# Performance work log

Measured on AMD Instinct MI355X. Metric: run time of the kernel, lower is better.

## Reference

```python
import jax, jax.numpy as jnp
import numpy as np

NUM_GROUPS = 32
EPS = 1e-6


def setup_inputs() -> dict:
    key = jax.random.key(0)
    ks = jax.random.split(key, 6)
    b, c, H, W = 4, 512, 64, 64
    scale = 1.0 / np.sqrt(c)
    return {
        "x": jax.random.normal(ks[0], (b, c, H, W), dtype=jnp.float32),
        "gn_w": jnp.ones((c,), jnp.float32),
        "gn_b": jnp.zeros((c,), jnp.float32),
        "wq": jax.random.normal(ks[1], (c, c), jnp.float32) * scale,
        "bq": jnp.zeros((c,), jnp.float32),
        "wk": jax.random.normal(ks[2], (c, c), jnp.float32) * scale,
        "bk": jnp.zeros((c,), jnp.float32),
        "wv": jax.random.normal(ks[3], (c, c), jnp.float32) * scale,
        "bv": jnp.zeros((c,), jnp.float32),
        "wp": jax.random.normal(ks[4], (c, c), jnp.float32) * scale,
        "bp": jnp.zeros((c,), jnp.float32),
    }


def _group_norm(x, gamma, beta):
    b, c, H, W = x.shape
    xg = x.reshape(b, NUM_GROUPS, c // NUM_GROUPS, H, W)
    mean = xg.mean(axis=(2, 3, 4), keepdims=True)
    var = xg.var(axis=(2, 3, 4), keepdims=True)
    xn = (xg - mean) * jax.lax.rsqrt(var + EPS)
    xn = xn.reshape(b, c, H, W)
    return xn * gamma[None, :, None, None] + beta[None, :, None, None]


def reference(x, gn_w, gn_b, wq, bq, wk, bk, wv, bv, wp, bp):
    b, c, H, W = x.shape
    h = _group_norm(x, gn_w, gn_b)  # (b,c,H,W)
    hf = h.reshape(b, c, H * W)  # (b,c,n)
    # 1x1 convs == per-pixel linear maps; weight layout [out,in]
    q = jnp.einsum('oc,bcn->bno', wq, hf) + bq  # (b,n,c)
    k = jnp.einsum('oc,bcn->bon', wk, hf) + bk[None, :, None]  # (b,c,n)
    v = jnp.einsum('oc,bcn->bon', wv, hf) + bv[None, :, None]  # (b,c,n)
    attn = jnp.einsum('bnc,bcm->bnm', q, k) * (int(c) ** (-0.5))
    attn = jax.nn.softmax(attn, axis=2)  # softmax over keys m
    # A = v @ attn^T  -> (b,c,n) where A[:, :, n] = sum_m v[:,:,m] attn[n,m]
    A = jnp.einsum('bcm,bnm->bcn', v, attn)
    A = jnp.einsum('oc,bcn->bon', wp, A) + bp[None, :, None]
    return x + A.reshape(b, c, H, W)
```

## Files before the change

kernel.cpp:

```cpp
#include <hip/hip_runtime.h>

#define BATCH 4
#define CCH 512
#define NPIX 4096
#define NGRP 32
#define GSZ 16
#define GN_EPS 1e-6f

typedef __attribute__((ext_vector_type(8))) short short8;
typedef __attribute__((ext_vector_type(8))) unsigned short ushort8;
typedef __attribute__((ext_vector_type(4))) unsigned short ushort4v;
typedef __attribute__((ext_vector_type(4))) float f32x4;

__device__ inline unsigned short f2bf(float f) {
  unsigned u = __float_as_uint(f);
  unsigned r = u + 0x7fffu + ((u >> 16) & 1u);
  return (unsigned short)(r >> 16);
}
__device__ inline float bf2f(unsigned short us) {
  return __uint_as_float(((unsigned)us) << 16);
}

__global__ __launch_bounds__(256) void gn_stats(const float* __restrict__ x,
                                                float* __restrict__ stats) {
  int bg = blockIdx.x;
  const f32x4* base = (const f32x4*)(x + (size_t)bg * (GSZ * NPIX));
  float s = 0.f, ss = 0.f;
  const int n4 = GSZ * NPIX / 4;
  for (int i = threadIdx.x; i < n4; i += 256) {
    f32x4 v = base[i];
    s += v.x + v.y + v.z + v.w;
    ss += v.x * v.x + v.y * v.y + v.z * v.z + v.w * v.w;
  }
  for (int off = 32; off > 0; off >>= 1) {
    s += __shfl_xor(s, off, 64);
    ss += __shfl_xor(ss, off, 64);
  }
  __shared__ float rs[4], rss[4];
  int lane = threadIdx.x & 63, wid = threadIdx.x >> 6;
  if (lane == 0) { rs[wid] = s; rss[wid] = ss; }
  __syncthreads();
  if (threadIdx.x == 0) {
    float S = rs[0] + rs[1] + rs[2] + rs[3];
    float SS = rss[0] + rss[1] + rss[2] + rss[3];
    const float inv = 1.f / (float)(GSZ * NPIX);
    float mean = S * inv;
    float var = SS * inv - mean * mean;
    stats[bg * 2] = mean;
    stats[bg * 2 + 1] = rsqrtf(var + GN_EPS);
  }
}

__global__ __launch_bounds__(256) void gn_apply_t(const float* __restrict__ x,
                                                  const float* __restrict__ stats,
                                                  const float* __restrict__ gw,
                                                  const float* __restrict__ gb,
                                                  unsigned short* __restrict__ hT) {
  __shared__ float tile[64][65];
  int b = blockIdx.z, c0 = blockIdx.y * 64, n0 = blockIdx.x * 64;
  int t = threadIdx.x;
  int tc4 = t & 15, tr = t >> 4;
  const float* xb = x + ((size_t)b * CCH + c0) * NPIX + n0;
#pragma unroll
  for (int j = 0; j < 4; ++j) {
    int row = tr + j * 16;
    int c = c0 + row;
    float mean = stats[((size_t)b * NGRP + (c >> 4)) * 2];
    float rstd = stats[((size_t)b * NGRP + (c >> 4)) * 2 + 1];
    float ga = gw[c] * rstd;
    float be = gb[c] - mean * ga;
    f32x4 v = *(const f32x4*)(xb + (size_t)row * NPIX + tc4 * 4);
    tile[row][tc4 * 4 + 0] = v.x * ga + be;
    tile[row][tc4 * 4 + 1] = v.y * ga + be;
    tile[row][tc4 * 4 + 2] = v.z * ga + be;
    tile[row][tc4 * 4 + 3] = v.w * ga + be;
  }
  __syncthreads();
  int cc = t & 7, nr = t >> 3;
  unsigned short* outp = hT + ((size_t)b * NPIX + n0) * CCH + c0;
#pragma unroll
  for (int j = 0; j < 2; ++j) {
    int n = nr + j * 32;
    ushort8 pk;
#pragma unroll
    for (int i = 0; i < 8; ++i) pk[i] = f2bf(tile[cc * 8 + i][n]);
    *(ushort8*)(outp + (size_t)n * CCH + cc * 8) = pk;
  }
}

__global__ __launch_bounds__(256) void f32_to_bf16(const float* __restrict__ src,
                                                   unsigned short* __restrict__ dst,
                                                   int n4) {
  int i = blockIdx.x * 256 + threadIdx.x;
  if (i < n4) {
    f32x4 v = ((const f32x4*)src)[i];
    ushort4v o;
    o.x = f2bf(v.x); o.y = f2bf(v.y); o.z = f2bf(v.z); o.w = f2bf(v.w);
    ((ushort4v*)dst)[i] = o;
  }
}

template <int BIAS_MODE, int OUT_BF16, int RESID, int SWZ>
__global__ __launch_bounds__(256, 2) void gemm_bt(
    const unsigned short* __restrict__ A, const unsigned short* __restrict__ B,
    void* __restrict__ Cv, const float* __restrict__ bias,
    const float* __restrict__ resid, int M, int N, int K, int lda, int ldb,
    int ldc, long sA, long sB, long sC, long sR, float scale) {
  __shared__ __align__(16) unsigned short lA[128][40];
  __shared__ __align__(16) unsigned short lB[128][40];
  const int t = threadIdx.x;
  const int lane = t & 63, w = t >> 6;
  const int wr = w >> 1, wc = w & 1;
  const int fr = lane & 15, kg = lane >> 4;

  unsigned orig = blockIdx.x + gridDim.x * (blockIdx.y + gridDim.y * blockIdx.z);
  unsigned nwg = gridDim.x * gridDim.y * gridDim.z;
  unsigned tid = (orig & 7) * (nwg >> 3) + (orig >> 3);
  int mt, ntl, bz;
  if (SWZ == 2) {
    unsigned bx = tid % gridDim.x, r = tid / gridDim.x;
    ntl = (int)bx;
    mt = (int)(r % gridDim.y);
    bz = (int)(r / gridDim.y);
  } else {
    unsigned bx = tid % gridDim.x, r = tid / gridDim.x;
    mt = (int)bx;
    ntl = (int)(r % gridDim.y);
    bz = (int)(r / gridDim.y);
  }
  const int m0 = mt * 128, n0 = ntl * 128;

  const unsigned short* Abz = A + (long)bz * sA;
  const unsigned short* Bbz = B + (long)bz * sB;
  const int srow = t >> 1, skc = (t & 1) * 16;
  const unsigned short* gA = Abz + (size_t)(m0 + srow) * lda + skc;
  const unsigned short* gB = Bbz + (size_t)(n0 + srow) * ldb + skc;

  short8 a0X = *(const short8*)(gA);
  short8 a1X = *(const short8*)(gA + 8);
  short8 b0X = *(const short8*)(gB);
  short8 b1X = *(const short8*)(gB + 8);
  short8 a0Y = *(const short8*)(gA + 32);
  short8 a1Y = *(const short8*)(gA + 40);
  short8 b0Y = *(const short8*)(gB + 32);
  short8 b1Y = *(const short8*)(gB + 40);

  f32x4 acc[4][4];
  const f32x4 zero = {0.f, 0.f, 0.f, 0.f};
#pragma unroll
  for (int m = 0; m < 4; ++m)
#pragma unroll
    for (int n = 0; n < 4; ++n) acc[m][n] = zero;

  const int NT = K >> 5;
#define COMPUTE()                                                             \
  do {                                                                        \
    short8 af[4], bfr[4];                                                     \
    _Pragma("unroll") for (int m = 0; m < 4; ++m) af[m] =                     \
        *(const short8*)&lA[wr * 64 + m * 16 + fr][kg * 8];                   \
    _Pragma("unroll") for (int n = 0; n < 4; ++n) bfr[n] =                    \
        *(const short8*)&lB[wc * 64 + n * 16 + fr][kg * 8];                   \
    _Pragma("unroll") for (int m = 0; m < 4; ++m)                             \
        _Pragma("unroll") for (int n = 0; n < 4; ++n) acc[m][n] =             \
            __builtin_amdgcn_mfma_f32_16x16x32_bf16(af[m], bfr[n],            \
                                                    acc[m][n], 0, 0, 0);      \
  } while (0)

  for (int it = 0; it < NT; it += 2) {
    __syncthreads();
    *(short8*)&lA[srow][skc] = a0X;
    *(short8*)&lA[srow][skc + 8] = a1X;
    *(short8*)&lB[srow][skc] = b0X;
    *(short8*)&lB[srow][skc + 8] = b1X;
    if (it + 2 < NT) {
      a0X = *(const short8*)(gA + (it + 2) * 32);
      a1X = *(const short8*)(gA + (it + 2) * 32 + 8);
      b0X = *(const short8*)(gB + (it + 2) * 32);
      b1X = *(const short8*)(gB + (it + 2) * 32 + 8);
    }
    __syncthreads();
    COMPUTE();
    __syncthreads();
    *(short8*)&lA[srow][skc] = a0Y;
    *(short8*)&lA[srow][skc + 8] = a1Y;
    *(short8*)&lB[srow][skc] = b0Y;
    *(short8*)&lB[srow][skc + 8] = b1Y;
    if (it + 3 < NT) {
      a0Y = *(const short8*)(gA + (it + 3) * 32);
      a1Y = *(const short8*)(gA + (it + 3) * 32 + 8);
      b0Y = *(const short8*)(gB + (it + 3) * 32);
      b1Y = *(const short8*)(gB + (it + 3) * 32 + 8);
    }
    __syncthreads();
    COMPUTE();
  }
#undef COMPUTE

  const int rowbase = m0 + wr * 64 + kg * 4;
  const int colbase = n0 + wc * 64 + fr;
#pragma unroll
  for (int m = 0; m < 4; ++m) {
#pragma unroll
    for (int n = 0; n < 4; ++n) {
      int col = colbase + n * 16;
#pragma unroll
      for (int r = 0; r < 4; ++r) {
        int row = rowbase + m * 16 + r;
        float v = acc[m][n][r] * scale;
        if (BIAS_MODE == 1) v += bias[row];
        if (BIAS_MODE == 2) v += bias[col];
        if (RESID) v += resid[(size_t)bz * sR + (size_t)row * ldc + col];
        size_t idx = (size_t)bz * sC + (size_t)row * ldc + col;
        if (OUT_BF16)
          ((unsigned short*)Cv)[idx] = f2bf(v);
        else
          ((float*)Cv)[idx] = v;
      }
    }
  }
}

__global__ __launch_bounds__(512, 2) void attn_fused(
    const unsigned short* __restrict__ qg, const unsigned short* __restrict__ kgl,
    const unsigned short* __restrict__ vg, unsigned short* __restrict__ og,
    float scale) {
  __shared__ __align__(16) unsigned short Qs[64 * 512];
  __shared__ __align__(16) unsigned short Ck[2][16384];
  __shared__ __align__(16) unsigned short Ps[64 * 128];
  __shared__ float lred[2][32][4];
  __shared__ float linv[64];

  const int t = threadIdx.x;
  const int lane = t & 63;
  const int wid = t >> 6;
  const int wq = wid >> 2, wc = wid & 3;
  const int fr = lane & 15, kgp = lane >> 4;

  unsigned logical = ((unsigned)blockIdx.x & 7) * 32 + ((unsigned)blockIdx.x >> 3);
  const int bz = (int)(logical >> 6), qt = (int)(logical & 63);
  const size_t BS = (size_t)NPIX * CCH;
  const unsigned short* qb = qg + (size_t)bz * BS + (size_t)qt * 64 * CCH;
  const unsigned short* kb = kgl + (size_t)bz * BS;
  const unsigned short* vb = vg + (size_t)bz * BS;

  {
    const int row = t >> 3, c0 = (t & 7) * 64;
    const unsigned short* src = qb + (size_t)row * CCH + c0;
    const int sw = (row & 7) << 3;
#pragma unroll
    for (int i = 0; i < 8; ++i)
      *(short8*)&Qs[row * 512 + ((c0 + i * 8) ^ sw)] = *(const short8*)(src + i * 8);
  }

  const int krow = t >> 2, kseg = t & 3;
  const int kswz = (krow & 7) << 3;
  const unsigned short* gK = kb + (size_t)krow * CCH + kseg * 32;
  const unsigned short* gV = vb + (size_t)t * NPIX;

  short8 R0, R1, R2, R3;
#define LOADK(mt_, cc_)                                                       \
  do { const unsigned short* g = gK + (size_t)(mt_) * (128 * CCH) + (cc_) * 128; \
    R0 = *(const short8*)(g); R1 = *(const short8*)(g + 8);                   \
    R2 = *(const short8*)(g + 16); R3 = *(const short8*)(g + 24); } while (0)
#define LOADV(mt_, vc_)                                                       \
  do { const unsigned short* g = gV + (mt_) * 128 + (vc_) * 32;               \
    R0 = *(const short8*)(g); R1 = *(const short8*)(g + 8);                   \
    R2 = *(const short8*)(g + 16); R3 = *(const short8*)(g + 24); } while (0)
#define WRITEK(buf_)                                                          \
  do { unsigned short* d = &Ck[buf_][krow * 128];                             \
    *(short8*)(d + ((kseg * 32 + 0) ^ kswz)) = R0;                            \
    *(short8*)(d + ((kseg * 32 + 8) ^ kswz)) = R1;                            \
    *(short8*)(d + ((kseg * 32 + 16) ^ kswz)) = R2;                           \
    *(short8*)(d + ((kseg * 32 + 24) ^ kswz)) = R3; } while (0)
#define WRITEV(buf_)                                                          \
  do { unsigned short* d = &Ck[buf_][t * 8];                                  \
    *(short8*)(d + 0 * 4096) = R0; *(short8*)(d + 1 * 4096) = R1;             \
    *(short8*)(d + 2 * 4096) = R2; *(short8*)(d + 3 * 4096) = R3; } while (0)

#define PHASE_BAR()                                                           \
  do {                                                                        \
    __builtin_amdgcn_sched_barrier(0);                                        \
    asm volatile("s_waitcnt lgkmcnt(0)" ::: "memory");                        \
    __builtin_amdgcn_s_barrier();                                             \
    __builtin_amdgcn_sched_barrier(0);                                        \
  } while (0)

  f32x4 oa[2][8];
  const f32x4 zero = {0.f, 0.f, 0.f, 0.f};
#pragma unroll
  for (int i = 0; i < 2; ++i)
#pragma unroll
    for (int j = 0; j < 8; ++j) oa[i][j] = zero;
  f32x4 racc0 = zero, racc1 = zero;

  LOADK(0, 0);
  for (int mt = 0; mt < 32; ++mt) {
    f32x4 s00 = zero, s01 = zero, s10 = zero, s11 = zero;
#pragma unroll
    for (int ph = 0; ph < 8; ++ph) {
      const int buf = ph & 1;
      if (ph < 4) WRITEK(buf); else WRITEV(buf);
      if (ph < 3) { LOADK(mt, ph + 1); }
      else if (ph == 3) { LOADV(mt, 0); }
      else if (ph < 7) { LOADV(mt, ph - 3); }
      else { if (mt + 1 < 32) LOADK(mt + 1, 0); }
      PHASE_BAR();
      if (ph < 4) {
        __builtin_amdgcn_s_setprio(1);
#pragma unroll
        for (int kk = 0; kk < 4; ++kk) {
          const int q0 = wq * 32 + fr, q1 = wq * 32 + 16 + fr;
          const int col = ph * 128 + kk * 32 + kgp * 8;
          short8 a0 = *(const short8*)&Qs[q0 * 512 + ((col) ^ ((q0 & 7) << 3))];
          short8 a1 = *(const short8*)&Qs[q1 * 512 + ((col) ^ ((q1 & 7) << 3))];
          const int m0r = wc * 32 + fr, m1r = wc * 32 + 16 + fr;
          short8 b0 = *(const short8*)&Ck[buf][m0r * 128 +
                      ((kk * 32 + kgp * 8) ^ ((m0r & 7) << 3))];
          short8 b1 = *(const short8*)&Ck[buf][m1r * 128 +
                      ((kk * 32 + kgp * 8) ^ ((m1r & 7) << 3))];
          s00 = __builtin_amdgcn_mfma_f32_16x16x32_bf16(a0, b0, s00, 0, 0, 0);
          s01 = __builtin_amdgcn_mfma_f32_16x16x32_bf16(a0, b1, s01, 0, 0, 0);
          s10 = __builtin_amdgcn_mfma_f32_16x16x32_bf16(a1, b0, s10, 0, 0, 0);
          s11 = __builtin_amdgcn_mfma_f32_16x16x32_bf16(a1, b1, s11, 0, 0, 0);
        }
        __builtin_amdgcn_s_setprio(0);
        if (ph == 3) {
          f32x4 p00, p01, p10, p11;
#pragma unroll
          for (int r = 0; r < 4; ++r) {
            p00[r] = __expf(s00[r] * scale);
            p01[r] = __expf(s01[r] * scale);
            p10[r] = __expf(s10[r] * scale);
            p11[r] = __expf(s11[r] * scale);
          }
          f32x4 rs0 = p00 + p01, rs1 = p10 + p11;
#pragma unroll
          for (int off = 1; off <= 8; off <<= 1) {
#pragma unroll
            for (int r = 0; r < 4; ++r) {
              rs0[r] += __shfl_xor(rs0[r], off, 64);
              rs1[r] += __shfl_xor(rs1[r], off, 64);
            }
          }
          racc0 += rs0;
          racc1 += rs1;
#pragma unroll
          for (int r = 0; r < 4; ++r) {
            const int qa = wq * 32 + kgp * 4 + r;
            const int qbr = wq * 32 + 16 + kgp * 4 + r;
            const int swa = (qa & 7) << 3, swb = (qbr & 7) << 3;
            Ps[qa * 128 + ((wc * 32 + fr) ^ swa)] = f2bf(p00[r]);
            Ps[qa * 128 + ((wc * 32 + 16 + fr) ^ swa)] = f2bf(p01[r]);
            Ps[qbr * 128 + ((wc * 32 + fr) ^ swb)] = f2bf(p10[r]);
            Ps[qbr * 128 + ((wc * 32 + 16 + fr) ^ swb)] = f2bf(p11[r]);
          }
        }
      } else {
        const int vc = ph - 4;
        const int q0 = wq * 32 + fr, q1 = wq * 32 + 16 + fr;
        short8 pa0 = *(const short8*)&Ps[q0 * 128 +
                     ((vc * 32 + kgp * 8) ^ ((q0 & 7) << 3))];
        short8 pa1 = *(const short8*)&Ps[q1 * 128 +
                     ((vc * 32 + kgp * 8) ^ ((q1 & 7) << 3))];
        __builtin_amdgcn_s_setprio(1);
#pragma unroll
        for (int fb = 0; fb < 8; ++fb) {
          const int c = wc * 128 + fb * 16 + fr;
          short8 bv = *(const short8*)&Ck[buf][kgp * 4096 + c * 8];
          oa[0][fb] = __builtin_amdgcn_mfma_f32_16x16x32_bf16(pa0, bv, oa[0][fb], 0, 0, 0);
          oa[1][fb] = __builtin_amdgcn_mfma_f32_16x16x32_bf16(pa1, bv, oa[1][fb], 0, 0, 0);
        }
        __builtin_amdgcn_s_setprio(0);
      }
    }
  }
#undef LOADK
#undef LOADV
#undef WRITEK
#undef WRITEV
#undef PHASE_BAR

  __syncthreads();
  if (fr == 0) {
#pragma unroll
    for (int r = 0; r < 4; ++r) {
      lred[wq][kgp * 4 + r][wc] = racc0[r];
      lred[wq][16 + kgp * 4 + r][wc] = racc1[r];
    }
  }
  __syncthreads();
  if (t < 64) {
    float s = lred[t >> 5][t & 31][0] + lred[t >> 5][t & 31][1] +
              lred[t >> 5][t & 31][2] + lred[t >> 5][t & 31][3];
    linv[t] = 1.f / s;
  }
  __syncthreads();
#pragma unroll
  for (int i = 0; i < 2; ++i) {
    f32x4 li = *(const f32x4*)&linv[wq * 32 + i * 16 + kgp * 4];
#pragma unroll
    for (int fb = 0; fb < 8; ++fb) {
#pragma unroll
      for (int r = 0; r < 4; ++r) {
        const int q = wq * 32 + i * 16 + kgp * 4 + r;
        const int col = wc * 128 + fb * 16 + fr;
        Qs[q * 512 + (col ^ ((q & 7) << 3))] = f2bf(oa[i][fb][r] * li[r]);
      }
    }
  }
  __syncthreads();
  {
    const int row = t >> 3, c0 = (t & 7) * 64;
    const int sw = (row & 7) << 3;
    unsigned short* dst = og + (size_t)bz * BS + ((size_t)qt * 64 + row) * CCH + c0;
#pragma unroll
    for (int i = 0; i < 8; ++i)
      *(short8*)(dst + i * 8) = *(const short8*)&Qs[row * 512 + ((c0 + i * 8) ^ sw)];
  }
}

extern "C" void kernel_launch(void* const* d_in, const int* in_sizes, int n_in,
                              void* d_out, int out_size, void* d_ws, size_t ws_size,
                              hipStream_t stream) {
  const float* x = (const float*)d_in[0];
  const float* gnw = (const float*)d_in[1];
  const float* gnb = (const float*)d_in[2];
  const float* wq = (const float*)d_in[3];
  const float* bq = (const float*)d_in[4];
  const float* wk = (const float*)d_in[5];
  const float* bk = (const float*)d_in[6];
  const float* wv = (const float*)d_in[7];
  const float* bv = (const float*)d_in[8];
  const float* wp = (const float*)d_in[9];
  const float* bp = (const float*)d_in[10];
  float* out = (float*)d_out;

  const size_t BS = (size_t)NPIX * CCH;

  char* ws = (char*)d_ws;
  float* stats = (float*)ws;
  unsigned short* hT = (unsigned short*)(ws + 1024);
  unsigned short* Abuf = hT;
  unsigned short* qb = hT + BATCH * BS;
  unsigned short* kTb = qb + BATCH * BS;
  unsigned short* vb = kTb + BATCH * BS;
  unsigned short* wqb = vb + BATCH * BS;
  unsigned short* wkb = wqb + CCH * CCH;
  unsigned short* wvb = wkb + CCH * CCH;
  unsigned short* wpb = wvb + CCH * CCH;
  size_t need = (size_t)((char*)(wpb + CCH * CCH) - ws);
  if (ws_size < need) return;

  f32_to_bf16<<<256, 256, 0, stream>>>(wq, wqb, CCH * CCH / 4);
  f32_to_bf16<<<256, 256, 0, stream>>>(wk, wkb, CCH * CCH / 4);
  f32_to_bf16<<<256, 256, 0, stream>>>(wv, wvb, CCH * CCH / 4);
  f32_to_bf16<<<256, 256, 0, stream>>>(wp, wpb, CCH * CCH / 4);

  gn_stats<<<BATCH * NGRP, 256, 0, stream>>>(x, stats);
  gn_apply_t<<<dim3(NPIX / 64, CCH / 64, BATCH), 256, 0, stream>>>(x, stats, gnw,
                                                                   gnb, hT);

  gemm_bt<2, 1, 0, 2><<<dim3(4, 32, BATCH), 256, 0, stream>>>(
      hT, wqb, qb, bq, nullptr, NPIX, CCH, CCH, CCH, CCH, CCH, (long)BS, 0,
      (long)BS, 0, 1.f);
  gemm_bt<2, 1, 0, 2><<<dim3(4, 32, BATCH), 256, 0, stream>>>(
      hT, wkb, kTb, bk, nullptr, NPIX, CCH, CCH, CCH, CCH, CCH, (long)BS, 0,
      (long)BS, 0, 1.f);
  gemm_bt<1, 1, 0, 0><<<dim3(4, 32, BATCH), 256, 0, stream>>>(
      wvb, hT, vb, bv, nullptr, CCH, NPIX, CCH, CCH, CCH, NPIX, 0, (long)BS,
      (long)BS, 0, 1.f);

  const float sscale = 0.044194173824159216f;
  attn_fused<<<BATCH * 64, 512, 0, stream>>>(qb, kTb, vb, Abuf, sscale);

  gemm_bt<1, 0, 1, 0><<<dim3(4, 32, BATCH), 256, 0, stream>>>(
      wpb, Abuf, out, bp, x, CCH, NPIX, CCH, CCH, CCH, NPIX, 0, (long)BS,
      (long)BS, (long)BS, 1.f);
}
```

Measured before the change: 336.3 us.

## Shrink attention query tile to 32 rows with 256-thread blocks

Restructures the fused attention kernel to process 32 query rows per block with 4 waves instead of 64 rows with 8 waves, launching 512 blocks instead of 256. Each wave now owns a 32-key slice for QK^T and a 64-channel slice (in two halves) for PV, with K staged in 64-channel chunks and V staged in 8 smaller phases. The aim is to fill more CUs with less LDS per block. The cost is that K/V tiles are reloaded from global or L2 twice as often in total, and there are more barriers per tile.

```diff
diff --git a/kernel.cpp b/kernel.cpp
--- a/kernel.cpp
+++ b/kernel.cpp
@@ -220,62 +220,54 @@
   }
 }
 
-__global__ __launch_bounds__(512, 2) void attn_fused(
+__global__ __launch_bounds__(256, 2) void attn_fused(
     const unsigned short* __restrict__ qg, const unsigned short* __restrict__ kgl,
     const unsigned short* __restrict__ vg, unsigned short* __restrict__ og,
     float scale) {
-  __shared__ __align__(16) unsigned short Qs[64 * 512];
-  __shared__ __align__(16) unsigned short Ck[2][16384];
-  __shared__ __align__(16) unsigned short Ps[64 * 128];
-  __shared__ float lred[2][32][4];
-  __shared__ float linv[64];
+  __shared__ __align__(16) unsigned short Qs[32 * 512];
+  __shared__ __align__(16) unsigned short Ck[2][8192];
+  __shared__ __align__(16) unsigned short Ps[32 * 128];
+  __shared__ float lred[32][4];
+  __shared__ float linv[32];
 
   const int t = threadIdx.x;
   const int lane = t & 63;
-  const int wid = t >> 6;
-  const int wq = wid >> 2, wc = wid & 3;
+  const int w = t >> 6;
   const int fr = lane & 15, kgp = lane >> 4;
 
-  unsigned logical = ((unsigned)blockIdx.x & 7) * 32 + ((unsigned)blockIdx.x >> 3);
-  const int bz = (int)(logical >> 6), qt = (int)(logical & 63);
+  unsigned logical = ((unsigned)blockIdx.x & 7) * 64 + ((unsigned)blockIdx.x >> 3);
+  const int bz = (int)(logical >> 7), qt = (int)(logical & 127);
   const size_t BS = (size_t)NPIX * CCH;
-  const unsigned short* qb = qg + (size_t)bz * BS + (size_t)qt * 64 * CCH;
+  const unsigned short* qb = qg + (size_t)bz * BS + (size_t)qt * 32 * CCH;
   const unsigned short* kb = kgl + (size_t)bz * BS;
   const unsigned short* vb = vg + (size_t)bz * BS;
 
-  {
-    const int row = t >> 3, c0 = (t & 7) * 64;
-    const unsigned short* src = qb + (size_t)row * CCH + c0;
-    const int sw = (row & 7) << 3;
-#pragma unroll
-    for (int i = 0; i < 8; ++i)
-      *(short8*)&Qs[row * 512 + ((c0 + i * 8) ^ sw)] = *(const short8*)(src + i * 8);
-  }
-
-  const int krow = t >> 2, kseg = t & 3;
-  const int kswz = (krow & 7) << 3;
-  const unsigned short* gK = kb + (size_t)krow * CCH + kseg * 32;
+  const int krow = t >> 1;
+  const int kch4 = (t & 1) * 4;
+  const int kswz = krow & 7;
+  const unsigned short* gK = kb + (size_t)krow * CCH + (t & 1) * 32;
   const unsigned short* gV = vb + (size_t)t * NPIX;
 
   short8 R0, R1, R2, R3;
-#define LOADK(mt_, cc_)                                                       \
-  do { const unsigned short* g = gK + (size_t)(mt_) * (128 * CCH) + (cc_) * 128; \
+#define LOADK(mt_, sub_)                                                      \
+  do { const unsigned short* g = gK + (size_t)(mt_) * (128 * CCH) + (sub_) * 64; \
     R0 = *(const short8*)(g); R1 = *(const short8*)(g + 8);                   \
     R2 = *(const short8*)(g + 16); R3 = *(const short8*)(g + 24); } while (0)
-#define LOADV(mt_, vc_)                                                       \
-  do { const unsigned short* g = gV + (mt_) * 128 + (vc_) * 32;               \
+#define LOADV(mt_, vph_)                                                      \
+  do { const unsigned short* g = gV + (size_t)((vph_) & 1) * (256 * NPIX) +   \
+        (mt_) * 128 + ((vph_) >> 1) * 32;                                     \
     R0 = *(const short8*)(g); R1 = *(const short8*)(g + 8);                   \
     R2 = *(const short8*)(g + 16); R3 = *(const short8*)(g + 24); } while (0)
 #define WRITEK(buf_)                                                          \
-  do { unsigned short* d = &Ck[buf_][krow * 128];                             \
-    *(short8*)(d + ((kseg * 32 + 0) ^ kswz)) = R0;                            \
-    *(short8*)(d + ((kseg * 32 + 8) ^ kswz)) = R1;                            \
-    *(short8*)(d + ((kseg * 32 + 16) ^ kswz)) = R2;                           \
-    *(short8*)(d + ((kseg * 32 + 24) ^ kswz)) = R3; } while (0)
+  do { unsigned short* d = &Ck[buf_][krow * 64];                              \
+    *(short8*)(d + (((kch4 + 0) ^ kswz) << 3)) = R0;                          \
+    *(short8*)(d + (((kch4 + 1) ^ kswz) << 3)) = R1;                          \
+    *(short8*)(d + (((kch4 + 2) ^ kswz) << 3)) = R2;                          \
+    *(short8*)(d + (((kch4 + 3) ^ kswz) << 3)) = R3; } while (0)
 #define WRITEV(buf_)                                                          \
   do { unsigned short* d = &Ck[buf_][t * 8];                                  \
-    *(short8*)(d + 0 * 4096) = R0; *(short8*)(d + 1 * 4096) = R1;             \
-    *(short8*)(d + 2 * 4096) = R2; *(short8*)(d + 3 * 4096) = R3; } while (0)
+    *(short8*)(d + 0 * 2048) = R0; *(short8*)(d + 1 * 2048) = R1;             \
+    *(short8*)(d + 2 * 2048) = R2; *(short8*)(d + 3 * 2048) = R3; } while (0)
 
 #define PHASE_BAR()                                                           \
   do {                                                                        \
@@ -285,93 +277,123 @@
     __builtin_amdgcn_sched_barrier(0);                                        \
   } while (0)
 
-  f32x4 oa[2][8];
+  LOADK(0, 0);
+  {
+    const int row = t >> 3, c0 = (t & 7) * 64;
+    const unsigned short* src = qb + (size_t)row * CCH + c0;
+    const int sw = (row & 7) << 3;
+#pragma unroll
+    for (int i = 0; i < 8; ++i)
+      *(short8*)&Qs[row * 512 + ((c0 + i * 8) ^ sw)] = *(const short8*)(src + i * 8);
+  }
+
+  f32x4 s_acc[2][2], o_acc[2][2][4], racc[2];
   const f32x4 zero = {0.f, 0.f, 0.f, 0.f};
 #pragma unroll
-  for (int i = 0; i < 2; ++i)
-#pragma unroll
-    for (int j = 0; j < 8; ++j) oa[i][j] = zero;
-  f32x4 racc0 = zero, racc1 = zero;
-
-  LOADK(0, 0);
+  for (int i = 0; i < 2; ++i) {
+    racc[i] = zero;
+#pragma unroll
+    for (int n = 0; n < 2; ++n) s_acc[i][n] = zero;
+#pragma unroll
+    for (int h = 0; h < 2; ++h)
+#pragma unroll
+      for (int n = 0; n < 4; ++n) o_acc[h][i][n] = zero;
+  }
+
+  short8 pa[2];
+
   for (int mt = 0; mt < 32; ++mt) {
-    f32x4 s00 = zero, s01 = zero, s10 = zero, s11 = zero;
-#pragma unroll
-    for (int ph = 0; ph < 8; ++ph) {
-      const int buf = ph & 1;
-      if (ph < 4) WRITEK(buf); else WRITEV(buf);
-      if (ph < 3) { LOADK(mt, ph + 1); }
-      else if (ph == 3) { LOADV(mt, 0); }
-      else if (ph < 7) { LOADV(mt, ph - 3); }
-      else { if (mt + 1 < 32) LOADK(mt + 1, 0); }
+#pragma unroll
+    for (int sub = 0; sub < 8; ++sub) {
+      const int buf = sub & 1;
+      WRITEK(buf);
+      if (sub < 7) LOADK(mt, sub + 1);
+      else         LOADV(mt, 0);
       PHASE_BAR();
-      if (ph < 4) {
-        __builtin_amdgcn_s_setprio(1);
-#pragma unroll
-        for (int kk = 0; kk < 4; ++kk) {
-          const int q0 = wq * 32 + fr, q1 = wq * 32 + 16 + fr;
-          const int col = ph * 128 + kk * 32 + kgp * 8;
-          short8 a0 = *(const short8*)&Qs[q0 * 512 + ((col) ^ ((q0 & 7) << 3))];
-          short8 a1 = *(const short8*)&Qs[q1 * 512 + ((col) ^ ((q1 & 7) << 3))];
-          const int m0r = wc * 32 + fr, m1r = wc * 32 + 16 + fr;
-          short8 b0 = *(const short8*)&Ck[buf][m0r * 128 +
-                      ((kk * 32 + kgp * 8) ^ ((m0r & 7) << 3))];
-          short8 b1 = *(const short8*)&Ck[buf][m1r * 128 +
-                      ((kk * 32 + kgp * 8) ^ ((m1r & 7) << 3))];
-          s00 = __builtin_amdgcn_mfma_f32_16x16x32_bf16(a0, b0, s00, 0, 0, 0);
-          s01 = __builtin_amdgcn_mfma_f32_16x16x32_bf16(a0, b1, s01, 0, 0, 0);
-          s10 = __builtin_amdgcn_mfma_f32_16x16x32_bf16(a1, b0, s10, 0, 0, 0);
-          s11 = __builtin_amdgcn_mfma_f32_16x16x32_bf16(a1, b1, s11, 0, 0, 0);
+      __builtin_amdgcn_s_setprio(1);
+#pragma unroll
+      for (int kk = 0; kk < 2; ++kk) {
+        short8 a[2], b[2];
+#pragma unroll
+        for (int i = 0; i < 2; ++i) {
+          const int q = i * 16 + fr;
+          const int col = sub * 64 + kk * 32 + kgp * 8;
+          a[i] = *(const short8*)&Qs[q * 512 + (col ^ ((q & 7) << 3))];
         }
-        __builtin_amdgcn_s_setprio(0);
-        if (ph == 3) {
-          f32x4 p00, p01, p10, p11;
+#pragma unroll
+        for (int n = 0; n < 2; ++n) {
+          const int m = w * 32 + n * 16 + fr;
+          b[n] = *(const short8*)&Ck[buf][m * 64 +
+                 (((kk * 4 + kgp) ^ (m & 7)) << 3)];
+        }
+#pragma unroll
+        for (int i = 0; i < 2; ++i)
+#pragma unroll
+          for (int n = 0; n < 2; ++n)
+            s_acc[i][n] = __builtin_amdgcn_mfma_f32_16x16x32_bf16(
+                a[i], b[n], s_acc[i][n], 0, 0, 0);
+      }
+      __builtin_amdgcn_s_setprio(0);
+      if (sub == 7) {
+#pragma unroll
+        for (int i = 0; i < 2; ++i) {
+          f32x4 p0, p1;
 #pragma unroll
           for (int r = 0; r < 4; ++r) {
-            p00[r] = __expf(s00[r] * scale);
-            p01[r] = __expf(s01[r] * scale);
-            p10[r] = __expf(s10[r] * scale);
-            p11[r] = __expf(s11[r] * scale);
+            p0[r] = __expf(s_acc[i][0][r] * scale);
+            p1[r] = __expf(s_acc[i][1][r] * scale);
           }
-          f32x4 rs0 = p00 + p01, rs1 = p10 + p11;
-#pragma unroll
-          for (int off = 1; off <= 8; off <<= 1) {
-#pragma unroll
-            for (int r = 0; r < 4; ++r) {
-              rs0[r] += __shfl_xor(rs0[r], off, 64);
-              rs1[r] += __shfl_xor(rs1[r], off, 64);
-            }
+          f32x4 rs = p0 + p1;
+#pragma unroll
+          for (int off = 1; off <= 8; off <<= 1)
+#pragma unroll
+            for (int r = 0; r < 4; ++r) rs[r] += __shfl_xor(rs[r], off, 64);
+          racc[i] += rs;
+#pragma unroll
+          for (int r = 0; r < 4; ++r) {
+            const int q = i * 16 + kgp * 4 + r;
+            const int m0e = w * 32 + fr;
+            const int m1e = w * 32 + 16 + fr;
+            Ps[q * 128 + ((((m0e >> 3) ^ (q & 7)) << 3) + (m0e & 7))] = f2bf(p0[r]);
+            Ps[q * 128 + ((((m1e >> 3) ^ (q & 7)) << 3) + (m1e & 7))] = f2bf(p1[r]);
           }
-          racc0 += rs0;
-          racc1 += rs1;
-#pragma unroll
-          for (int r = 0; r < 4; ++r) {
-            const int qa = wq * 32 + kgp * 4 + r;
-            const int qbr = wq * 32 + 16 + kgp * 4 + r;
-            const int swa = (qa & 7) << 3, swb = (qbr & 7) << 3;
-            Ps[qa * 128 + ((wc * 32 + fr) ^ swa)] = f2bf(p00[r]);
-            Ps[qa * 128 + ((wc * 32 + 16 + fr) ^ swa)] = f2bf(p01[r]);
-            Ps[qbr * 128 + ((wc * 32 + fr) ^ swb)] = f2bf(p10[r]);
-            Ps[qbr * 128 + ((wc * 32 + 16 + fr) ^ swb)] = f2bf(p11[r]);
-          }
+          s_acc[i][0] = zero;
+          s_acc[i][1] = zero;
         }
-      } else {
-        const int vc = ph - 4;
-        const int q0 = wq * 32 + fr, q1 = wq * 32 + 16 + fr;
-        short8 pa0 = *(const short8*)&Ps[q0 * 128 +
-                     ((vc * 32 + kgp * 8) ^ ((q0 & 7) << 3))];
-        short8 pa1 = *(const short8*)&Ps[q1 * 128 +
-                     ((vc * 32 + kgp * 8) ^ ((q1 & 7) << 3))];
-        __builtin_amdgcn_s_setprio(1);
-#pragma unroll
-        for (int fb = 0; fb < 8; ++fb) {
-          const int c = wc * 128 + fb * 16 + fr;
-          short8 bv = *(const short8*)&Ck[buf][kgp * 4096 + c * 8];
-          oa[0][fb] = __builtin_amdgcn_mfma_f32_16x16x32_bf16(pa0, bv, oa[0][fb], 0, 0, 0);
-          oa[1][fb] = __builtin_amdgcn_mfma_f32_16x16x32_bf16(pa1, bv, oa[1][fb], 0, 0, 0);
+      }
+    }
+#pragma unroll
+    for (int vph = 0; vph < 8; ++vph) {
+      const int buf = vph & 1;
+      const int h = vph & 1, mc = vph >> 1;
+      WRITEV(buf);
+      if (vph < 7) LOADV(mt, vph + 1);
+      else if (mt + 1 < 32) LOADK(mt + 1, 0);
+      PHASE_BAR();
+      if (h == 0) {
+#pragma unroll
+        for (int i = 0; i < 2; ++i) {
+          const int q = i * 16 + fr;
+          pa[i] = *(const short8*)&Ps[q * 128 +
+                  (((mc * 4 + kgp) ^ (q & 7)) << 3)];
         }
-        __builtin_amdgcn_s_setprio(0);
       }
+      __builtin_amdgcn_s_setprio(1);
+      {
+        short8 b[4];
+#pragma unroll
+        for (int n = 0; n < 4; ++n) {
+          const int cl = w * 64 + n * 16 + fr;
+          b[n] = *(const short8*)&Ck[buf][(kgp << 11) + cl * 8];
+        }
+#pragma unroll
+        for (int i = 0; i < 2; ++i)
+#pragma unroll
+          for (int n = 0; n < 4; ++n)
+            o_acc[h][i][n] = __builtin_amdgcn_mfma_f32_16x16x32_bf16(
+                pa[i], b[n], o_acc[h][i][n], 0, 0, 0);
+      }
+      __builtin_amdgcn_s_setprio(0);
     }
   }
 #undef LOADK
@@ -383,28 +405,30 @@
   __syncthreads();
   if (fr == 0) {
 #pragma unroll
-    for (int r = 0; r < 4; ++r) {
-      lred[wq][kgp * 4 + r][wc] = racc0[r];
-      lred[wq][16 + kgp * 4 + r][wc] = racc1[r];
-    }
+    for (int i = 0; i < 2; ++i)
+#pragma unroll
+      for (int r = 0; r < 4; ++r)
+        lred[i * 16 + kgp * 4 + r][w] = racc[i][r];
   }
   __syncthreads();
-  if (t < 64) {
-    float s = lred[t >> 5][t & 31][0] + lred[t >> 5][t & 31][1] +
-              lred[t >> 5][t & 31][2] + lred[t >> 5][t & 31][3];
+  if (t < 32) {
+    float s = lred[t][0] + lred[t][1] + lred[t][2] + lred[t][3];
     linv[t] = 1.f / s;
   }
   __syncthreads();
 #pragma unroll
   for (int i = 0; i < 2; ++i) {
-    f32x4 li = *(const f32x4*)&linv[wq * 32 + i * 16 + kgp * 4];
-#pragma unroll
-    for (int fb = 0; fb < 8; ++fb) {
-#pragma unroll
-      for (int r = 0; r < 4; ++r) {
-        const int q = wq * 32 + i * 16 + kgp * 4 + r;
-        const int col = wc * 128 + fb * 16 + fr;
-        Qs[q * 512 + (col ^ ((q & 7) << 3))] = f2bf(oa[i][fb][r] * li[r]);
+    f32x4 li = *(const f32x4*)&linv[i * 16 + kgp * 4];
+#pragma unroll
+    for (int h = 0; h < 2; ++h) {
+#pragma unroll
+      for (int n = 0; n < 4; ++n) {
+#pragma unroll
+        for (int r = 0; r < 4; ++r) {
+          const int q = i * 16 + kgp * 4 + r;
+          const int c = h * 256 + w * 64 + n * 16 + fr;
+          Qs[q * 512 + (c ^ ((q & 7) << 3))] = f2bf(o_acc[h][i][n][r] * li[r]);
+        }
       }
     }
   }
@@ -412,7 +436,7 @@
   {
     const int row = t >> 3, c0 = (t & 7) * 64;
     const int sw = (row & 7) << 3;
-    unsigned short* dst = og + (size_t)bz * BS + ((size_t)qt * 64 + row) * CCH + c0;
+    unsigned short* dst = og + (size_t)bz * BS + ((size_t)qt * 32 + row) * CCH + c0;
 #pragma unroll
     for (int i = 0; i < 8; ++i)
       *(short8*)(dst + i * 8) = *(const short8*)&Qs[row * 512 + ((c0 + i * 8) ^ sw)];
@@ -471,7 +495,7 @@
       (long)BS, 0, 1.f);
 
   const float sscale = 0.044194173824159216f;
-  attn_fused<<<BATCH * 64, 512, 0, stream>>>(qb, kTb, vb, Abuf, sscale);
+  attn_fused<<<512, 256, 0, stream>>>(qb, kTb, vb, Abuf, sscale);
 
   gemm_bt<1, 0, 1, 0><<<dim3(4, 32, BATCH), 256, 0, stream>>>(
       wpb, Abuf, out, bp, x, CCH, NPIX, CCH, CCH, CCH, NPIX, 0, (long)BS,
```

Result: slower. 457.5 us (+36.0%).

## Double attention block to 1024 threads with one 16-row query slice per wave

Applied to the files above, without the earlier changes.

The fused attention kernel now launches 1024 threads (16 waves) per block instead of 512, and each wave handles 16 query rows rather than 32, halving per-wave accumulators and MFMA work. K/V staging loads are redistributed so each thread moves two 16-byte chunks per phase instead of four, and the first K prefetch is issued before the Q tile load. The row-sum scratch now reuses the Ps buffer to save LDS. The aim is more latency hiding and less register pressure per wave. The cost is more waves per barrier, each doing less MFMA work between barriers, and the same LDS footprint, which limits blocks per CU.

```diff
diff --git a/kernel.cpp b/kernel.cpp
--- a/kernel.cpp
+++ b/kernel.cpp
@@ -220,20 +220,19 @@
   }
 }
 
-__global__ __launch_bounds__(512, 2) void attn_fused(
+__global__ __launch_bounds__(1024, 4) void attn_fused(
     const unsigned short* __restrict__ qg, const unsigned short* __restrict__ kgl,
     const unsigned short* __restrict__ vg, unsigned short* __restrict__ og,
     float scale) {
   __shared__ __align__(16) unsigned short Qs[64 * 512];
   __shared__ __align__(16) unsigned short Ck[2][16384];
   __shared__ __align__(16) unsigned short Ps[64 * 128];
-  __shared__ float lred[2][32][4];
-  __shared__ float linv[64];
 
   const int t = threadIdx.x;
   const int lane = t & 63;
   const int wid = t >> 6;
-  const int wq = wid >> 2, wc = wid & 3;
+  const int wq = wid >> 2;
+  const int wc = wid & 3;
   const int fr = lane & 15, kgp = lane >> 4;
 
   unsigned logical = ((unsigned)blockIdx.x & 7) * 32 + ((unsigned)blockIdx.x >> 3);
@@ -243,39 +242,27 @@
   const unsigned short* kb = kgl + (size_t)bz * BS;
   const unsigned short* vb = vg + (size_t)bz * BS;
 
-  {
-    const int row = t >> 3, c0 = (t & 7) * 64;
-    const unsigned short* src = qb + (size_t)row * CCH + c0;
-    const int sw = (row & 7) << 3;
-#pragma unroll
-    for (int i = 0; i < 8; ++i)
-      *(short8*)&Qs[row * 512 + ((c0 + i * 8) ^ sw)] = *(const short8*)(src + i * 8);
-  }
-
-  const int krow = t >> 2, kseg = t & 3;
-  const int kswz = (krow & 7) << 3;
-  const unsigned short* gK = kb + (size_t)krow * CCH + kseg * 32;
-  const unsigned short* gV = vb + (size_t)t * NPIX;
-
-  short8 R0, R1, R2, R3;
-#define LOADK(mt_, cc_)                                                       \
-  do { const unsigned short* g = gK + (size_t)(mt_) * (128 * CCH) + (cc_) * 128; \
-    R0 = *(const short8*)(g); R1 = *(const short8*)(g + 8);                   \
-    R2 = *(const short8*)(g + 16); R3 = *(const short8*)(g + 24); } while (0)
+  const int krow = t >> 3, kg0 = (t & 7) * 2;
+  const int kx = krow & 7;
+  const unsigned short* gKbase = kb + (size_t)krow * CCH + kg0 * 8;
+  const int vgr = t >> 8, vc0 = (2 * t) & 511;
+  const unsigned short* gV0 = vb + (size_t)vc0 * NPIX + vgr * 8;
+  const unsigned short* gV1 = vb + (size_t)(vc0 + 1) * NPIX + vgr * 8;
+
+  short8 R0, R1;
+#define LOADK(mt_, ph_)                                                       \
+  do { const unsigned short* g = gKbase + (size_t)(mt_) * (128 * CCH) + (ph_)*128; \
+    R0 = *(const short8*)(g); R1 = *(const short8*)(g + 8); } while (0)
 #define LOADV(mt_, vc_)                                                       \
-  do { const unsigned short* g = gV + (mt_) * 128 + (vc_) * 32;               \
-    R0 = *(const short8*)(g); R1 = *(const short8*)(g + 8);                   \
-    R2 = *(const short8*)(g + 16); R3 = *(const short8*)(g + 24); } while (0)
+  do { const long m0v = (long)(mt_)*128 + (long)(vc_)*32;                     \
+    R0 = *(const short8*)(gV0 + m0v); R1 = *(const short8*)(gV1 + m0v); } while (0)
 #define WRITEK(buf_)                                                          \
   do { unsigned short* d = &Ck[buf_][krow * 128];                             \
-    *(short8*)(d + ((kseg * 32 + 0) ^ kswz)) = R0;                            \
-    *(short8*)(d + ((kseg * 32 + 8) ^ kswz)) = R1;                            \
-    *(short8*)(d + ((kseg * 32 + 16) ^ kswz)) = R2;                           \
-    *(short8*)(d + ((kseg * 32 + 24) ^ kswz)) = R3; } while (0)
+    *(short8*)(d + ((kg0 ^ kx) << 3)) = R0;                                   \
+    *(short8*)(d + (((kg0 + 1) ^ kx) << 3)) = R1; } while (0)
 #define WRITEV(buf_)                                                          \
-  do { unsigned short* d = &Ck[buf_][t * 8];                                  \
-    *(short8*)(d + 0 * 4096) = R0; *(short8*)(d + 1 * 4096) = R1;             \
-    *(short8*)(d + 2 * 4096) = R2; *(short8*)(d + 3 * 4096) = R3; } while (0)
+  do { unsigned short* d = &Ck[buf_][vgr * 4096 + vc0 * 8];                   \
+    *(short8*)(d) = R0; *(short8*)(d + 8) = R1; } while (0)
 
 #define PHASE_BAR()                                                           \
   do {                                                                        \
@@ -285,90 +272,84 @@
     __builtin_amdgcn_sched_barrier(0);                                        \
   } while (0)
 
-  f32x4 oa[2][8];
+  LOADK(0, 0);
+  {
+    const int row = t >> 4, c0 = (t & 15) * 32;
+    const unsigned short* src = qb + (size_t)row * CCH + c0;
+    const int sw = (row & 7) << 3;
+#pragma unroll
+    for (int i = 0; i < 4; ++i)
+      *(short8*)&Qs[row * 512 + ((c0 + i * 8) ^ sw)] = *(const short8*)(src + i * 8);
+  }
+
+  f32x4 s_acc[2], oa[8], racc;
   const f32x4 zero = {0.f, 0.f, 0.f, 0.f};
-#pragma unroll
-  for (int i = 0; i < 2; ++i)
-#pragma unroll
-    for (int j = 0; j < 8; ++j) oa[i][j] = zero;
-  f32x4 racc0 = zero, racc1 = zero;
-
-  LOADK(0, 0);
+  s_acc[0] = zero; s_acc[1] = zero; racc = zero;
+#pragma unroll
+  for (int j = 0; j < 8; ++j) oa[j] = zero;
+
   for (int mt = 0; mt < 32; ++mt) {
-    f32x4 s00 = zero, s01 = zero, s10 = zero, s11 = zero;
 #pragma unroll
     for (int ph = 0; ph < 8; ++ph) {
       const int buf = ph & 1;
       if (ph < 4) WRITEK(buf); else WRITEV(buf);
-      if (ph < 3) { LOADK(mt, ph + 1); }
-      else if (ph == 3) { LOADV(mt, 0); }
-      else if (ph < 7) { LOADV(mt, ph - 3); }
+      if (ph < 3)       LOADK(mt, ph + 1);
+      else if (ph == 3) LOADV(mt, 0);
+      else if (ph < 7)  LOADV(mt, ph - 3);
       else { if (mt + 1 < 32) LOADK(mt + 1, 0); }
       PHASE_BAR();
       if (ph < 4) {
+        const int q0 = wq * 16 + fr;
+        const int qx = (q0 & 7) << 3;
+        const int m0r = wc * 32 + fr, m1r = wc * 32 + 16 + fr;
+        const int mx0 = (m0r & 7) << 3, mx1 = (m1r & 7) << 3;
         __builtin_amdgcn_s_setprio(1);
 #pragma unroll
         for (int kk = 0; kk < 4; ++kk) {
-          const int q0 = wq * 32 + fr, q1 = wq * 32 + 16 + fr;
           const int col = ph * 128 + kk * 32 + kgp * 8;
-          short8 a0 = *(const short8*)&Qs[q0 * 512 + ((col) ^ ((q0 & 7) << 3))];
-          short8 a1 = *(const short8*)&Qs[q1 * 512 + ((col) ^ ((q1 & 7) << 3))];
-          const int m0r = wc * 32 + fr, m1r = wc * 32 + 16 + fr;
+          short8 a = *(const short8*)&Qs[q0 * 512 + (col ^ qx)];
           short8 b0 = *(const short8*)&Ck[buf][m0r * 128 +
-                      ((kk * 32 + kgp * 8) ^ ((m0r & 7) << 3))];
+                      ((kk * 32 + kgp * 8) ^ mx0)];
           short8 b1 = *(const short8*)&Ck[buf][m1r * 128 +
-                      ((kk * 32 + kgp * 8) ^ ((m1r & 7) << 3))];
-          s00 = __builtin_amdgcn_mfma_f32_16x16x32_bf16(a0, b0, s00, 0, 0, 0);
-          s01 = __builtin_amdgcn_mfma_f32_16x16x32_bf16(a0, b1, s01, 0, 0, 0);
-          s10 = __builtin_amdgcn_mfma_f32_16x16x32_bf16(a1, b0, s10, 0, 0, 0);
-          s11 = __builtin_amdgcn_mfma_f32_16x16x32_bf16(a1, b1, s11, 0, 0, 0);
+                      ((kk * 32 + kgp * 8) ^ mx1)];
+          s_acc[0] = __builtin_amdgcn_mfma_f32_16x16x32_bf16(a, b0, s_acc[0], 0, 0, 0);
+          s_acc[1] = __builtin_amdgcn_mfma_f32_16x16x32_bf16(a, b1, s_acc[1], 0, 0, 0);
         }
         __builtin_amdgcn_s_setprio(0);
         if (ph == 3) {
-          f32x4 p00, p01, p10, p11;
+          f32x4 p0, p1;
 #pragma unroll
           for (int r = 0; r < 4; ++r) {
-            p00[r] = __expf(s00[r] * scale);
-            p01[r] = __expf(s01[r] * scale);
-            p10[r] = __expf(s10[r] * scale);
-            p11[r] = __expf(s11[r] * scale);
+            p0[r] = __expf(s_acc[0][r] * scale);
+            p1[r] = __expf(s_acc[1][r] * scale);
           }
-          f32x4 rs0 = p00 + p01, rs1 = p10 + p11;
-#pragma unroll
-          for (int off = 1; off <= 8; off <<= 1) {
-#pragma unroll
-            for (int r = 0; r < 4; ++r) {
-              rs0[r] += __shfl_xor(rs0[r], off, 64);
-              rs1[r] += __shfl_xor(rs1[r], off, 64);
-            }
+          f32x4 rs = p0 + p1;
+#pragma unroll
+          for (int off = 1; off <= 8; off <<= 1)
+#pragma unroll
+            for (int r = 0; r < 4; ++r) rs[r] += __shfl_xor(rs[r], off, 64);
+          racc += rs;
+#pragma unroll
+          for (int r = 0; r < 4; ++r) {
+            const int qa = wq * 16 + kgp * 4 + r;
+            const int swa = (qa & 7) << 3;
+            Ps[qa * 128 + ((wc * 32 + fr) ^ swa)] = f2bf(p0[r]);
+            Ps[qa * 128 + ((wc * 32 + 16 + fr) ^ swa)] = f2bf(p1[r]);
           }
-          racc0 += rs0;
-          racc1 += rs1;
-#pragma unroll
-          for (int r = 0; r < 4; ++r) {
-            const int qa = wq * 32 + kgp * 4 + r;
-            const int qbr = wq * 32 + 16 + kgp * 4 + r;
-            const int swa = (qa & 7) << 3, swb = (qbr & 7) << 3;
-            Ps[qa * 128 + ((wc * 32 + fr) ^ swa)] = f2bf(p00[r]);
-            Ps[qa * 128 + ((wc * 32 + 16 + fr) ^ swa)] = f2bf(p01[r]);
-            Ps[qbr * 128 + ((wc * 32 + fr) ^ swb)] = f2bf(p10[r]);
-            Ps[qbr * 128 + ((wc * 32 + 16 + fr) ^ swb)] = f2bf(p11[r]);
-          }
+          s_acc[0] = zero;
+          s_acc[1] = zero;
         }
       } else {
         const int vc = ph - 4;
-        const int q0 = wq * 32 + fr, q1 = wq * 32 + 16 + fr;
-        short8 pa0 = *(const short8*)&Ps[q0 * 128 +
-                     ((vc * 32 + kgp * 8) ^ ((q0 & 7) << 3))];
-        short8 pa1 = *(const short8*)&Ps[q1 * 128 +
-                     ((vc * 32 + kgp * 8) ^ ((q1 & 7) << 3))];
+        const int q0 = wq * 16 + fr;
+        short8 pa = *(const short8*)&Ps[q0 * 128 +
+                    ((vc * 32 + kgp * 8) ^ ((q0 & 7) << 3))];
         __builtin_amdgcn_s_setprio(1);
 #pragma unroll
         for (int fb = 0; fb < 8; ++fb) {
           const int c = wc * 128 + fb * 16 + fr;
           short8 bv = *(const short8*)&Ck[buf][kgp * 4096 + c * 8];
-          oa[0][fb] = __builtin_amdgcn_mfma_f32_16x16x32_bf16(pa0, bv, oa[0][fb], 0, 0, 0);
-          oa[1][fb] = __builtin_amdgcn_mfma_f32_16x16x32_bf16(pa1, bv, oa[1][fb], 0, 0, 0);
+          oa[fb] = __builtin_amdgcn_mfma_f32_16x16x32_bf16(pa, bv, oa[fb], 0, 0, 0);
         }
         __builtin_amdgcn_s_setprio(0);
       }
@@ -381,40 +362,39 @@
 #undef PHASE_BAR
 
   __syncthreads();
+  float* lredf = (float*)Ps;
+  float* linv = lredf + 256;
   if (fr == 0) {
 #pragma unroll
-    for (int r = 0; r < 4; ++r) {
-      lred[wq][kgp * 4 + r][wc] = racc0[r];
-      lred[wq][16 + kgp * 4 + r][wc] = racc1[r];
-    }
+    for (int r = 0; r < 4; ++r)
+      lredf[(wq * 16 + kgp * 4 + r) * 4 + wc] = racc[r];
   }
   __syncthreads();
   if (t < 64) {
-    float s = lred[t >> 5][t & 31][0] + lred[t >> 5][t & 31][1] +
-              lred[t >> 5][t & 31][2] + lred[t >> 5][t & 31][3];
+    float s = lredf[t * 4] + lredf[t * 4 + 1] + lredf[t * 4 + 2] + lredf[t * 4 + 3];
     linv[t] = 1.f / s;
   }
   __syncthreads();
-#pragma unroll
-  for (int i = 0; i < 2; ++i) {
-    f32x4 li = *(const f32x4*)&linv[wq * 32 + i * 16 + kgp * 4];
+  {
+    f32x4 li = *(const f32x4*)&linv[wq * 16 + kgp * 4];
+    __syncthreads();
 #pragma unroll
     for (int fb = 0; fb < 8; ++fb) {
 #pragma unroll
       for (int r = 0; r < 4; ++r) {
-        const int q = wq * 32 + i * 16 + kgp * 4 + r;
+        const int q = wq * 16 + kgp * 4 + r;
         const int col = wc * 128 + fb * 16 + fr;
-        Qs[q * 512 + (col ^ ((q & 7) << 3))] = f2bf(oa[i][fb][r] * li[r]);
+        Qs[q * 512 + (col ^ ((q & 7) << 3))] = f2bf(oa[fb][r] * li[r]);
       }
     }
   }
   __syncthreads();
   {
-    const int row = t >> 3, c0 = (t & 7) * 64;
+    const int row = t >> 4, c0 = (t & 15) * 32;
     const int sw = (row & 7) << 3;
     unsigned short* dst = og + (size_t)bz * BS + ((size_t)qt * 64 + row) * CCH + c0;
 #pragma unroll
-    for (int i = 0; i < 8; ++i)
+    for (int i = 0; i < 4; ++i)
       *(short8*)(dst + i * 8) = *(const short8*)&Qs[row * 512 + ((c0 + i * 8) ^ sw)];
   }
 }
@@ -471,7 +451,7 @@
       (long)BS, 0, 1.f);
 
   const float sscale = 0.044194173824159216f;
-  attn_fused<<<BATCH * 64, 512, 0, stream>>>(qb, kTb, vb, Abuf, sscale);
+  attn_fused<<<BATCH * 64, 1024, 0, stream>>>(qb, kTb, vb, Abuf, sscale);
 
   gemm_bt<1, 0, 1, 0><<<dim3(4, 32, BATCH), 256, 0, stream>>>(
       wpb, Abuf, out, bp, x, CCH, NPIX, CCH, CCH, CCH, NPIX, 0, (long)BS,
```

Measured after the change: 454.2 us. 35.0% more time.
